# Performance work log

Hardware: AMD Instinct MI355X
Metric: run time of the kernel (lower is better)

Reference implementation:

```python
import jax, jax.numpy as jnp
import numpy as np

D_MODEL = 768
N_HEAD = 12

def setup_inputs() -> dict:
    key = jax.random.key(0)
    ks = jax.random.split(key, 5)
    B, T, C = 2, 2048, D_MODEL
    s = 1.0 / np.sqrt(C)
    x = jax.random.normal(ks[0], (B, T, C), dtype=jnp.float32)
    W_attn = jax.random.normal(ks[1], (C, 3 * C), dtype=jnp.float32) * s
    b_attn = jnp.zeros((3 * C,), dtype=jnp.float32)
    W_proj = jax.random.normal(ks[2], (C, C), dtype=jnp.float32) * s
    b_proj = jnp.zeros((C,), dtype=jnp.float32)
    return {"x": x, "W_attn": W_attn, "b_attn": b_attn, "W_proj": W_proj, "b_proj": b_proj}

def reference(x, W_attn, b_attn, W_proj, b_proj):
    B, T, C = x.shape
    H, Dh = N_HEAD, C // N_HEAD
    qkv = x @ W_attn + b_attn  # [B,T,3C]
    q, k, v = jnp.split(qkv, 3, axis=-1)
    q = q.reshape(B, T, H, Dh).transpose(0, 2, 1, 3)  # [B,H,T,Dh]
    k = k.reshape(B, T, H, Dh).transpose(0, 2, 1, 3)
    v = v.reshape(B, T, H, Dh).transpose(0, 2, 1, 3)
    att = jnp.einsum('bhqd,bhkd->bhqk', q, k) * (1.0 / np.sqrt(Dh))
    mask = jnp.tril(jnp.ones((T, T), dtype=bool))  # causal
    att = jnp.where(mask, att, -jnp.inf)
    att = jax.nn.softmax(att, axis=-1)
    y = jnp.einsum('bhqk,bhkd->bhqd', att, v)
    y = y.transpose(0, 2, 1, 3).reshape(B, T, C)
    return y @ W_proj + b_proj
```

## Files before the change

### kernel.cpp

```cpp
#include <hip/hip_runtime.h>
#include <hip/hip_bf16.h>
#include <math.h>

#define BB 2
#define TT 2048
#define CC 768
#define HH 12
#define DD 64
#define KD 768
#define NCH 40

#define QSCALE 0.18033688011112044f
#define M0 32.0f

typedef __attribute__((ext_vector_type(8))) short bf16x8;
typedef __attribute__((ext_vector_type(4))) float f32x4;
typedef __attribute__((ext_vector_type(4))) float f32x4v;
typedef __attribute__((ext_vector_type(4))) ushort u16x4;

static __device__ __forceinline__ ushort f2bf(float f) {
  union { float f; unsigned u; } v; v.f = f;
  unsigned r = v.u + 0x7FFF + ((v.u >> 16) & 1);
  return (ushort)(r >> 16);
}
static __device__ __forceinline__ float bf2f(ushort u) {
  union { unsigned u; float f; } v; v.u = ((unsigned)u) << 16;
  return v.f;
}

#define NB_CVT 3072
#define NB_TA  1728
#define NB_TP  576

__global__ __launch_bounds__(256) void prep_fused(
    const float* __restrict__ x, ushort* __restrict__ xb,
    const float* __restrict__ Wa, ushort* __restrict__ Wat,
    const float* __restrict__ Wp, ushort* __restrict__ Wpt) {
  const int bid = blockIdx.x;
  const int tid = threadIdx.x;
  if (bid < NB_CVT) {
    const int i = bid * 256 + tid;
    f32x4v v = ((const f32x4v*)x)[i];
    u16x4 o;
    o.x = f2bf(v.x); o.y = f2bf(v.y); o.z = f2bf(v.z); o.w = f2bf(v.w);
    ((u16x4*)xb)[i] = o;
    return;
  }
  __shared__ float t[32][33];
  const float* W; ushort* Wt; int N, idx;
  if (bid < NB_CVT + NB_TA) { W = Wa; Wt = Wat; N = 3 * CC; idx = bid - NB_CVT; }
  else                      { W = Wp; Wt = Wpt; N = CC;     idx = bid - NB_CVT - NB_TA; }
  const int ntx = N / 32;
  const int n0 = (idx % ntx) * 32, k0 = (idx / ntx) * 32;
  const int tx = tid & 31, ty = tid >> 5;
#pragma unroll
  for (int j = 0; j < 32; j += 8)
    t[ty + j][tx] = W[(size_t)(k0 + ty + j) * N + n0 + tx];
  __syncthreads();
#pragma unroll
  for (int j = 0; j < 32; j += 8)
    Wt[(size_t)(n0 + ty + j) * KD + k0 + tx] = f2bf(t[tx][ty + j]);
}

__global__ __launch_bounds__(256) void gemm_mfma(
    const ushort* __restrict__ A, const ushort* __restrict__ Bt,
    const float* __restrict__ bias, int N, int mode,
    ushort* __restrict__ Qo, ushort* __restrict__ Ko, ushort* __restrict__ Vo,
    float* __restrict__ Of) {
  __shared__ ushort As[128 * 32];
  __shared__ ushort Bs[128 * 32];
  const int tid = threadIdx.x;
  const int w = tid >> 6, lane = tid & 63;
  const int wr = w >> 1, wc = w & 1;
  const int grp = lane >> 4, colk = lane & 15;
  const int bm = blockIdx.y * 128, bn = blockIdx.x * 128;

  f32x4 acc[4][4] = {};

  auto* AsL = (__attribute__((address_space(3))) char*)As;
  auto* BsL = (__attribute__((address_space(3))) char*)Bs;

  for (int k0 = 0; k0 < KD; k0 += 32) {
#pragma unroll
    for (int i = 0; i < 2; ++i) {
      const int idx = tid + i * 256;
      const int row = idx >> 2, g = idx & 3;
      const int eoff = (g * 8) ^ ((row & 3) << 3);
      const ushort* sa = A + (size_t)(bm + row) * KD + k0 + eoff;
      const ushort* sb = Bt + (size_t)(bn + row) * KD + k0 + eoff;
      __builtin_amdgcn_global_load_lds(
          (const __attribute__((address_space(1))) void*)sa,
          (__attribute__((address_space(3))) void*)(AsL + w * 1024 + i * 4096), 16, 0, 0);
      __builtin_amdgcn_global_load_lds(
          (const __attribute__((address_space(1))) void*)sb,
          (__attribute__((address_space(3))) void*)(BsL + w * 1024 + i * 4096), 16, 0, 0);
    }
    __syncthreads();

    bf16x8 af[4], bf[4];
    const int sw = (colk & 3) << 3;
#pragma unroll
    for (int m = 0; m < 4; ++m)
      af[m] = *(const bf16x8*)&As[(wr * 64 + m * 16 + colk) * 32 + ((grp * 8) ^ sw)];
#pragma unroll
    for (int n = 0; n < 4; ++n)
      bf[n] = *(const bf16x8*)&Bs[(wc * 64 + n * 16 + colk) * 32 + ((grp * 8) ^ sw)];
#pragma unroll
    for (int m = 0; m < 4; ++m)
#pragma unroll
      for (int n = 0; n < 4; ++n)
        acc[m][n] = __builtin_amdgcn_mfma_f32_16x16x32_bf16(af[m], bf[n], acc[m][n], 0, 0, 0);
    __syncthreads();
  }

#pragma unroll
  for (int m = 0; m < 4; ++m) {
    const int gro = bm + wr * 64 + m * 16 + grp * 4;
#pragma unroll
    for (int n = 0; n < 4; ++n) {
      const int col = bn + wc * 64 + n * 16 + colk;
      const float bv = bias[col];
#pragma unroll
      for (int j = 0; j < 4; ++j) {
        const int row = gro + j;
        float v = acc[m][n][j] + bv;
        if (mode == 0) {
          const int which = col / CC;
          const int c = col - which * CC;
          const int hh = c >> 6, d = c & 63;
          const int b = row >> 11, t = row & 2047;
          if (which == 0) v *= QSCALE;
          const ushort bvv = f2bf(v);
          if (which == 0)
            Qo[((size_t)((b * HH + hh) * TT + t)) * DD + d] = bvv;
          else if (which == 1)
            Ko[((size_t)((b * HH + hh) * TT + t)) * DD + d] = bvv;
          else
            Vo[((size_t)((b * HH + hh) * DD + d)) * TT + t] = bvv;
        } else {
          Of[(size_t)row * N + col] = v;
        }
      }
    }
  }
}

__global__ __launch_bounds__(512, 4) void attn_mfma(
    const ushort* __restrict__ Q, const ushort* __restrict__ K,
    const ushort* __restrict__ Vt, ushort* __restrict__ Po,
    float* __restrict__ Pl) {
  const int c = NCH - 1 - (int)blockIdx.x;
  int qq, ci;
  if (c < 4)       { qq = c;                               ci = 0; }
  else if (c < 12) { int o_ = c - 4;  qq = 4  + (o_ >> 1); ci = o_ & 1; }
  else if (c < 24) { int o_ = c - 12; qq = 8  + o_ / 3;    ci = o_ % 3; }
  else             { int o_ = c - 24; qq = 12 + (o_ >> 2); ci = o_ & 3; }
  const int h = blockIdx.y, b = blockIdx.z;
  const int bh = b * HH + h;
  const size_t hb = (size_t)bh * TT * DD;
  const int kbase = ci * 512;
  const int nt = min(8, 2 * (qq + 1) - ci * 8);

  __shared__ ushort Ks[64][72];
  __shared__ ushort Vs[64][72];
  __shared__ ushort Ps[8][16][72];

  const int tid = threadIdx.x;
  const int w = tid >> 6, lane = tid & 63;
  const int grp = lane >> 4, colk = lane & 15;
  const int q0w = qq * 128 + w * 16;
  const int qme = q0w + colk;

  const ushort* Kg = K + hb;
  const ushort* Vg = Vt + hb;

  bf16x8 qf[2];
  {
    const ushort* qp = Q + hb + (size_t)(q0w + colk) * DD + 8 * grp;
    qf[0] = *(const bf16x8*)(qp);
    qf[1] = *(const bf16x8*)(qp + 32);
  }

  f32x4 o[4] = {};
  float l = 0.f;

  const int srow = tid >> 3;
  const int scol = (tid & 7) * 8;

  {
    bf16x8 k0a = *(const bf16x8*)&Kg[(size_t)(kbase + srow) * DD + scol];
    bf16x8 v0a = *(const bf16x8*)&Vg[(size_t)srow * TT + kbase + scol];
    *(bf16x8*)&Ks[srow][scol] = k0a;
    *(bf16x8*)&Vs[srow][scol] = v0a;
  }
  __syncthreads();

  for (int it = 0; it < nt; ++it) {
    const int k0 = kbase + it * 64;
    const bool pfn = (it + 1 < nt);
    bf16x8 nk0, nv0;
    if (pfn) {
      nk0 = *(const bf16x8*)&Kg[(size_t)(k0 + 64 + srow) * DD + scol];
      nv0 = *(const bf16x8*)&Vg[(size_t)srow * TT + k0 + 64 + scol];
    }

    if (k0 <= q0w) {
      f32x4 s2[4] = {};
      __builtin_amdgcn_s_setprio(1);
#pragma unroll
      for (int kb = 0; kb < 4; ++kb) {
        bf16x8 kf0 = *(const bf16x8*)&Ks[16 * kb + colk][8 * grp];
        bf16x8 kf1 = *(const bf16x8*)&Ks[16 * kb + colk][32 + 8 * grp];
        s2[kb] = __builtin_amdgcn_mfma_f32_16x16x32_bf16(kf0, qf[0], s2[kb], 0, 0, 0);
        s2[kb] = __builtin_amdgcn_mfma_f32_16x16x32_bf16(kf1, qf[1], s2[kb], 0, 0, 0);
      }
      __builtin_amdgcn_s_setprio(0);

      if (k0 + 63 > q0w) {
#pragma unroll
        for (int kb = 0; kb < 4; ++kb)
#pragma unroll
          for (int r = 0; r < 4; ++r)
            if (k0 + 16 * kb + 4 * grp + r > qme) s2[kb][r] = -1e30f;
      }

#pragma unroll
      for (int kb = 0; kb < 4; ++kb) {
        const float p0 = exp2f(s2[kb][0] - M0);
        const float p1 = exp2f(s2[kb][1] - M0);
        const float p2 = exp2f(s2[kb][2] - M0);
        const float p3 = exp2f(s2[kb][3] - M0);
        l += (p0 + p1) + (p2 + p3);
        union { __hip_bfloat162 h2[2]; uint2 u2; } pk;
        pk.h2[0] = __float22bfloat162_rn(make_float2(p0, p1));
        pk.h2[1] = __float22bfloat162_rn(make_float2(p2, p3));
        *(uint2*)&Ps[w][colk][16 * kb + 4 * grp] = pk.u2;
      }

      bf16x8 pf0 = *(const bf16x8*)&Ps[w][colk][8 * grp];
      bf16x8 pf1 = *(const bf16x8*)&Ps[w][colk][32 + 8 * grp];
      __builtin_amdgcn_s_setprio(1);
#pragma unroll
      for (int n = 0; n < 4; ++n) {
        bf16x8 vf0 = *(const bf16x8*)&Vs[16 * n + colk][8 * grp];
        bf16x8 vf1 = *(const bf16x8*)&Vs[16 * n + colk][32 + 8 * grp];
        o[n] = __builtin_amdgcn_mfma_f32_16x16x32_bf16(pf0, vf0, o[n], 0, 0, 0);
        o[n] = __builtin_amdgcn_mfma_f32_16x16x32_bf16(pf1, vf1, o[n], 0, 0, 0);
      }
      __builtin_amdgcn_s_setprio(0);
    }

    if (pfn) {
      __syncthreads();
      *(bf16x8*)&Ks[srow][scol] = nk0;
      *(bf16x8*)&Vs[srow][scol] = nv0;
      __syncthreads();
    }
  }

  l += __shfl_xor(l, 16);
  l += __shfl_xor(l, 32);

  const size_t pbase = ((size_t)bh * NCH + c) * 128;
#pragma unroll
  for (int r = 0; r < 4; ++r) {
    const int row = w * 16 + grp * 4 + r;
#pragma unroll
    for (int n = 0; n < 4; ++n)
      Po[(pbase + row) * 64 + 16 * n + colk] = f2bf(o[n][r]);
  }
  if (grp == 0) Pl[pbase + w * 16 + colk] = l;
}

__global__ __launch_bounds__(256) void attn_merge(
    const ushort* __restrict__ Po, const float* __restrict__ Pl,
    ushort* __restrict__ Yb) {
  const int qq = blockIdx.x, h = blockIdx.y, b = blockIdx.z;
  const int bh = b * HH + h;
  const int qh = qq >> 1;
  const int gg = qh >> 2;
  const int nch = gg + 1;
  const int gb = (gg == 0) ? 0 : (gg == 1) ? 4 : (gg == 2) ? 12 : 24;
  const int cb = gb + nch * (qh - 4 * gg);
  const int rowo = (qq & 1) * 64;

  const int tid = threadIdx.x;
  const int row = tid >> 2;
  const int d0 = (tid & 3) * 16;

  float acc[16] = {};
  float lt = 0.f;
#pragma unroll
  for (int i = 0; i < 4; ++i) {
    if (i < nch) {
      const size_t pb = ((size_t)bh * NCH + cb + i) * 128 + rowo + row;
      lt += Pl[pb];
      const ushort* pp = Po + pb * 64 + d0;
      bf16x8 a = *(const bf16x8*)pp;
      bf16x8 bv = *(const bf16x8*)(pp + 8);
#pragma unroll
      for (int j = 0; j < 8; ++j) {
        acc[j] += bf2f((ushort)a[j]);
        acc[8 + j] += bf2f((ushort)bv[j]);
      }
    }
  }
  const float inv = 1.0f / lt;
  const int t = qq * 64 + row;
  ushort* yp = Yb + ((size_t)(b * TT) + t) * CC + h * DD + d0;
  bf16x8 o0, o1;
#pragma unroll
  for (int j = 0; j < 8; ++j) {
    o0[j] = (short)f2bf(acc[j] * inv);
    o1[j] = (short)f2bf(acc[8 + j] * inv);
  }
  *(bf16x8*)yp = o0;
  *(bf16x8*)(yp + 8) = o1;
}

extern "C" void kernel_launch(void* const* d_in, const int* in_sizes, int n_in,
                              void* d_out, int out_size, void* d_ws, size_t ws_size,
                              hipStream_t stream) {
  const float* x      = (const float*)d_in[0];
  const float* W_attn = (const float*)d_in[1];
  const float* b_attn = (const float*)d_in[2];
  const float* W_proj = (const float*)d_in[3];
  const float* b_proj = (const float*)d_in[4];
  float* out = (float*)d_out;

  const size_t per = (size_t)BB * TT * CC;
  ushort* Q   = (ushort*)d_ws;
  ushort* K   = Q + per;
  ushort* VtT = K + per;
  ushort* Yb  = VtT + per;
  ushort* Wpt = Yb + per;
  ushort* xb  = Wpt + (size_t)CC * CC;
  ushort* Wat = xb + per;
  ushort* Po  = xb;
  float*  Pl  = (float*)(Po + (size_t)BB * HH * NCH * 128 * 64);

  prep_fused<<<dim3(NB_CVT + NB_TA + NB_TP), 256, 0, stream>>>(
      x, xb, W_attn, Wat, W_proj, Wpt);

  gemm_mfma<<<dim3(3 * CC / 128, BB * TT / 128), 256, 0, stream>>>(
      xb, Wat, b_attn, 3 * CC, 0, Q, K, VtT, nullptr);
  attn_mfma<<<dim3(NCH, HH, BB), 512, 0, stream>>>(Q, K, VtT, Po, Pl);
  attn_merge<<<dim3(TT / 64, HH, BB), 256, 0, stream>>>(Po, Pl, Yb);
  gemm_mfma<<<dim3(CC / 128, BB * TT / 128), 256, 0, stream>>>(
      Yb, Wpt, b_proj, CC, 1, nullptr, nullptr, nullptr, out);
}
```

Before: 113.1 us.

## Fuse split-KV merge into attention kernel via last-block atomic counter

```diff
diff --git a/kernel.cpp b/kernel.cpp
--- a/kernel.cpp
+++ b/kernel.cpp
@@ -148,7 +148,8 @@
 __global__ __launch_bounds__(512, 4) void attn_mfma(
     const ushort* __restrict__ Q, const ushort* __restrict__ K,
     const ushort* __restrict__ Vt, ushort* __restrict__ Po,
-    float* __restrict__ Pl) {
+    float* __restrict__ Pl, int* __restrict__ cnt,
+    ushort* __restrict__ Yb) {
   const int c = NCH - 1 - (int)blockIdx.x;
   int qq, ci;
   if (c < 4)       { qq = c;                               ci = 0; }
@@ -164,6 +165,7 @@
   __shared__ ushort Ks[64][72];
   __shared__ ushort Vs[64][72];
   __shared__ ushort Ps[8][16][72];
+  __shared__ int lastFlag;
 
   const int tid = threadIdx.x;
   const int w = tid >> 6, lane = tid & 63;
@@ -261,6 +263,22 @@
   l += __shfl_xor(l, 16);
   l += __shfl_xor(l, 32);
 
+  const int nch = (qq >> 2) + 1;
+  if (nch == 1) {
+    float li[4];
+#pragma unroll
+    for (int r = 0; r < 4; ++r) li[r] = 1.0f / __shfl(l, grp * 4 + r);
+#pragma unroll
+    for (int r = 0; r < 4; ++r) {
+      const int t = qq * 128 + w * 16 + grp * 4 + r;
+      ushort* yp = Yb + ((size_t)(b * TT) + t) * CC + h * DD;
+#pragma unroll
+      for (int n = 0; n < 4; ++n)
+        yp[16 * n + colk] = f2bf(o[n][r] * li[r]);
+    }
+    return;
+  }
+
   const size_t pbase = ((size_t)bh * NCH + c) * 128;
 #pragma unroll
   for (int r = 0; r < 4; ++r) {
@@ -270,30 +288,28 @@
       Po[(pbase + row) * 64 + 16 * n + colk] = f2bf(o[n][r]);
   }
   if (grp == 0) Pl[pbase + w * 16 + colk] = l;
-}
-
-__global__ __launch_bounds__(256) void attn_merge(
-    const ushort* __restrict__ Po, const float* __restrict__ Pl,
-    ushort* __restrict__ Yb) {
-  const int qq = blockIdx.x, h = blockIdx.y, b = blockIdx.z;
-  const int bh = b * HH + h;
-  const int qh = qq >> 1;
-  const int gg = qh >> 2;
-  const int nch = gg + 1;
-  const int gb = (gg == 0) ? 0 : (gg == 1) ? 4 : (gg == 2) ? 12 : 24;
-  const int cb = gb + nch * (qh - 4 * gg);
-  const int rowo = (qq & 1) * 64;
-
-  const int tid = threadIdx.x;
-  const int row = tid >> 2;
+
+  __syncthreads();
+  if (tid == 0) {
+    __threadfence();
+    const int prev = atomicAdd(&cnt[bh * 16 + qq], 1);
+    lastFlag = (prev == nch - 1);
+  }
+  __syncthreads();
+  if (!lastFlag) return;
+  __threadfence();
+
+  const int gg = qq >> 2;
+  const int gb = (gg == 1) ? 4 : (gg == 2) ? 12 : 24;
+  const int cb = gb + nch * (qq - 4 * gg);
+  const int mrow = tid >> 2;
   const int d0 = (tid & 3) * 16;
-
   float acc[16] = {};
   float lt = 0.f;
 #pragma unroll
   for (int i = 0; i < 4; ++i) {
     if (i < nch) {
-      const size_t pb = ((size_t)bh * NCH + cb + i) * 128 + rowo + row;
+      const size_t pb = ((size_t)bh * NCH + cb + i) * 128 + mrow;
       lt += Pl[pb];
       const ushort* pp = Po + pb * 64 + d0;
       bf16x8 a = *(const bf16x8*)pp;
@@ -306,7 +322,7 @@
     }
   }
   const float inv = 1.0f / lt;
-  const int t = qq * 64 + row;
+  const int t = qq * 128 + mrow;
   ushort* yp = Yb + ((size_t)(b * TT) + t) * CC + h * DD + d0;
   bf16x8 o0, o1;
 #pragma unroll
@@ -338,14 +354,18 @@
   ushort* Wat = xb + per;
   ushort* Po  = xb;
   float*  Pl  = (float*)(Po + (size_t)BB * HH * NCH * 128 * 64);
+  int*    cnt = (int*)(Pl + (size_t)BB * HH * NCH * 128);
 
   prep_fused<<<dim3(NB_CVT + NB_TA + NB_TP), 256, 0, stream>>>(
       x, xb, W_attn, Wat, W_proj, Wpt);
 
   gemm_mfma<<<dim3(3 * CC / 128, BB * TT / 128), 256, 0, stream>>>(
       xb, Wat, b_attn, 3 * CC, 0, Q, K, VtT, nullptr);
-  attn_mfma<<<dim3(NCH, HH, BB), 512, 0, stream>>>(Q, K, VtT, Po, Pl);
-  attn_merge<<<dim3(TT / 64, HH, BB), 256, 0, stream>>>(Po, Pl, Yb);
+
+  hipMemsetAsync(cnt, 0, (size_t)BB * HH * 16 * sizeof(int), stream);
+
+  attn_mfma<<<dim3(NCH, HH, BB), 512, 0, stream>>>(Q, K, VtT, Po, Pl, cnt, Yb);
+
   gemm_mfma<<<dim3(CC / 128, BB * TT / 128), 256, 0, stream>>>(
       Yb, Wpt, b_proj, CC, 1, nullptr, nullptr, nullptr, out);
 }
```

After: 290.3 us. +156.6%, slower.

## Finalize single-chunk attention rows in-kernel and use narrower output-projection GEMM tiles

Applied to the files above, without the earlier changes.

```diff
diff --git a/kernel.cpp b/kernel.cpp
--- a/kernel.cpp
+++ b/kernel.cpp
@@ -64,9 +64,8 @@
 
 __global__ __launch_bounds__(256) void gemm_mfma(
     const ushort* __restrict__ A, const ushort* __restrict__ Bt,
-    const float* __restrict__ bias, int N, int mode,
-    ushort* __restrict__ Qo, ushort* __restrict__ Ko, ushort* __restrict__ Vo,
-    float* __restrict__ Of) {
+    const float* __restrict__ bias,
+    ushort* __restrict__ Qo, ushort* __restrict__ Ko, ushort* __restrict__ Vo) {
   __shared__ ushort As[128 * 32];
   __shared__ ushort Bs[128 * 32];
   const int tid = threadIdx.x;
@@ -74,6 +73,7 @@
   const int wr = w >> 1, wc = w & 1;
   const int grp = lane >> 4, colk = lane & 15;
   const int bm = blockIdx.y * 128, bn = blockIdx.x * 128;
+  const int N = 3 * CC;
 
   f32x4 acc[4][4] = {};
 
@@ -120,27 +120,89 @@
     for (int n = 0; n < 4; ++n) {
       const int col = bn + wc * 64 + n * 16 + colk;
       const float bv = bias[col];
+      const int which = col / CC;
+      const int ccc = col - which * CC;
+      const int hh = ccc >> 6, d = ccc & 63;
 #pragma unroll
       for (int j = 0; j < 4; ++j) {
         const int row = gro + j;
         float v = acc[m][n][j] + bv;
-        if (mode == 0) {
-          const int which = col / CC;
-          const int c = col - which * CC;
-          const int hh = c >> 6, d = c & 63;
-          const int b = row >> 11, t = row & 2047;
-          if (which == 0) v *= QSCALE;
-          const ushort bvv = f2bf(v);
-          if (which == 0)
-            Qo[((size_t)((b * HH + hh) * TT + t)) * DD + d] = bvv;
-          else if (which == 1)
-            Ko[((size_t)((b * HH + hh) * TT + t)) * DD + d] = bvv;
-          else
-            Vo[((size_t)((b * HH + hh) * DD + d)) * TT + t] = bvv;
-        } else {
-          Of[(size_t)row * N + col] = v;
-        }
-      }
+        const int b = row >> 11, t = row & 2047;
+        if (which == 0) v *= QSCALE;
+        const ushort bvv = f2bf(v);
+        if (which == 0)
+          Qo[((size_t)((b * HH + hh) * TT + t)) * DD + d] = bvv;
+        else if (which == 1)
+          Ko[((size_t)((b * HH + hh) * TT + t)) * DD + d] = bvv;
+        else
+          Vo[((size_t)((b * HH + hh) * DD + d)) * TT + t] = bvv;
+      }
+    }
+  }
+}
+
+__global__ __launch_bounds__(256) void gemm_n64(
+    const ushort* __restrict__ A, const ushort* __restrict__ Bt,
+    const float* __restrict__ bias, float* __restrict__ Of) {
+  __shared__ ushort As[128 * 32];
+  __shared__ ushort Bs[64 * 32];
+  const int tid = threadIdx.x;
+  const int w = tid >> 6, lane = tid & 63;
+  const int grp = lane >> 4, colk = lane & 15;
+  const int bm = blockIdx.y * 128, bn = blockIdx.x * 64;
+
+  f32x4 acc[2][4] = {};
+
+  auto* AsL = (__attribute__((address_space(3))) char*)As;
+  auto* BsL = (__attribute__((address_space(3))) char*)Bs;
+
+  for (int k0 = 0; k0 < KD; k0 += 32) {
+#pragma unroll
+    for (int i = 0; i < 2; ++i) {
+      const int idx = tid + i * 256;
+      const int row = idx >> 2, g = idx & 3;
+      const int eoff = (g * 8) ^ ((row & 3) << 3);
+      const ushort* sa = A + (size_t)(bm + row) * KD + k0 + eoff;
+      __builtin_amdgcn_global_load_lds(
+          (const __attribute__((address_space(1))) void*)sa,
+          (__attribute__((address_space(3))) void*)(AsL + w * 1024 + i * 4096), 16, 0, 0);
+    }
+    {
+      const int row = tid >> 2, g = tid & 3;
+      const int eoff = (g * 8) ^ ((row & 3) << 3);
+      const ushort* sb = Bt + (size_t)(bn + row) * KD + k0 + eoff;
+      __builtin_amdgcn_global_load_lds(
+          (const __attribute__((address_space(1))) void*)sb,
+          (__attribute__((address_space(3))) void*)(BsL + w * 1024), 16, 0, 0);
+    }
+    __syncthreads();
+
+    bf16x8 af[2], bf[4];
+    const int sw = (colk & 3) << 3;
+#pragma unroll
+    for (int m = 0; m < 2; ++m)
+      af[m] = *(const bf16x8*)&As[(w * 32 + m * 16 + colk) * 32 + ((grp * 8) ^ sw)];
+#pragma unroll
+    for (int n = 0; n < 4; ++n)
+      bf[n] = *(const bf16x8*)&Bs[(n * 16 + colk) * 32 + ((grp * 8) ^ sw)];
+#pragma unroll
+    for (int m = 0; m < 2; ++m)
+#pragma unroll
+      for (int n = 0; n < 4; ++n)
+        acc[m][n] = __builtin_amdgcn_mfma_f32_16x16x32_bf16(af[m], bf[n], acc[m][n], 0, 0, 0);
+    __syncthreads();
+  }
+
+#pragma unroll
+  for (int m = 0; m < 2; ++m) {
+    const int gro = bm + w * 32 + m * 16 + grp * 4;
+#pragma unroll
+    for (int n = 0; n < 4; ++n) {
+      const int col = bn + n * 16 + colk;
+      const float bv = bias[col];
+#pragma unroll
+      for (int j = 0; j < 4; ++j)
+        Of[(size_t)(gro + j) * CC + col] = acc[m][n][j] + bv;
     }
   }
 }
@@ -148,7 +210,7 @@
 __global__ __launch_bounds__(512, 4) void attn_mfma(
     const ushort* __restrict__ Q, const ushort* __restrict__ K,
     const ushort* __restrict__ Vt, ushort* __restrict__ Po,
-    float* __restrict__ Pl) {
+    float* __restrict__ Pl, ushort* __restrict__ Yb) {
   const int c = NCH - 1 - (int)blockIdx.x;
   int qq, ci;
   if (c < 4)       { qq = c;                               ci = 0; }
@@ -261,6 +323,21 @@
   l += __shfl_xor(l, 16);
   l += __shfl_xor(l, 32);
 
+  if (qq < 4) {
+    float li[4];
+#pragma unroll
+    for (int r = 0; r < 4; ++r) li[r] = 1.0f / __shfl(l, grp * 4 + r);
+#pragma unroll
+    for (int r = 0; r < 4; ++r) {
+      const int t = qq * 128 + w * 16 + grp * 4 + r;
+      ushort* yp = Yb + ((size_t)(b * TT) + t) * CC + h * DD;
+#pragma unroll
+      for (int n = 0; n < 4; ++n)
+        yp[16 * n + colk] = f2bf(o[n][r] * li[r]);
+    }
+    return;
+  }
+
   const size_t pbase = ((size_t)bh * NCH + c) * 128;
 #pragma unroll
   for (int r = 0; r < 4; ++r) {
@@ -275,12 +352,12 @@
 __global__ __launch_bounds__(256) void attn_merge(
     const ushort* __restrict__ Po, const float* __restrict__ Pl,
     ushort* __restrict__ Yb) {
-  const int qq = blockIdx.x, h = blockIdx.y, b = blockIdx.z;
+  const int qq = (int)blockIdx.x + 8, h = blockIdx.y, b = blockIdx.z;
   const int bh = b * HH + h;
   const int qh = qq >> 1;
   const int gg = qh >> 2;
   const int nch = gg + 1;
-  const int gb = (gg == 0) ? 0 : (gg == 1) ? 4 : (gg == 2) ? 12 : 24;
+  const int gb = (gg == 1) ? 4 : (gg == 2) ? 12 : 24;
   const int cb = gb + nch * (qh - 4 * gg);
   const int rowo = (qq & 1) * 64;
 
@@ -343,9 +420,9 @@
       x, xb, W_attn, Wat, W_proj, Wpt);
 
   gemm_mfma<<<dim3(3 * CC / 128, BB * TT / 128), 256, 0, stream>>>(
-      xb, Wat, b_attn, 3 * CC, 0, Q, K, VtT, nullptr);
-  attn_mfma<<<dim3(NCH, HH, BB), 512, 0, stream>>>(Q, K, VtT, Po, Pl);
-  attn_merge<<<dim3(TT / 64, HH, BB), 256, 0, stream>>>(Po, Pl, Yb);
-  gemm_mfma<<<dim3(CC / 128, BB * TT / 128), 256, 0, stream>>>(
-      Yb, Wpt, b_proj, CC, 1, nullptr, nullptr, nullptr, out);
-}
+      xb, Wat, b_attn, Q, K, VtT);
+  attn_mfma<<<dim3(NCH, HH, BB), 512, 0, stream>>>(Q, K, VtT, Po, Pl, Yb);
+  attn_merge<<<dim3(24, HH, BB), 256, 0, stream>>>(Po, Pl, Yb);
+  gemm_n64<<<dim3(CC / 64, BB * TT / 128), 256, 0, stream>>>(
+      Yb, Wpt, b_proj, out);
+}
```

After: 108.4 us. 1.04x faster.
